# Performance work log

Measured on AMD Instinct MI355X. Metric: run time of the kernel, lower is better.

The kernel has to match this reference:

```python
import jax, jax.numpy as jnp
from jax import lax
import numpy as np

B, T_FEAT, F_DIM = 200, 2048, 128
T_CHAR, VOCAB, EMB = 128, 5000, 150
H_FEAT, H_CHAR, HID, NCLS = 256, 200, 264, 8


def gru(x, h0, W, U, b):
    """Keras GRU (v2, reset_after=True). x: [B,T,D] -> final state [B,H]."""
    xw = jnp.einsum('btd,dh->bth', x, W) + b[0]  # input projection, [B,T,3H]
    def step(h, xt):
        rec = h @ U + b[1]                        # [B,3H]
        xz, xr, xh = jnp.split(xt, 3, axis=-1)
        rz, rr, rh = jnp.split(rec, 3, axis=-1)
        z = jax.nn.sigmoid(xz + rz)
        r = jax.nn.sigmoid(xr + rr)
        hh = jnp.tanh(xh + r * rh)
        h = z * h + (1.0 - z) * hh
        return h, None
    h, _ = lax.scan(step, h0, jnp.swapaxes(xw, 0, 1))  # scan over time
    return h


def setup_inputs() -> dict:
    key = jax.random.key(0)
    ks = jax.random.split(key, 24)
    s = lambda *sh: 1.0 / np.sqrt(sh[0])
    d = {
        'numerical_inputs': jax.random.normal(ks[0], (B, 32), jnp.float32),
        'feature_inputs': jax.random.normal(ks[1], (B, T_FEAT, F_DIM), jnp.float32),
        'char_inputs': jax.random.randint(ks[2], (B, T_CHAR), 0, VOCAB, jnp.int32),
        # char embedding table (truncated-normal in orig; normal*0.01 here)
        'emb': jax.random.normal(ks[3], (VOCAB, EMB), jnp.float32) * 0.01,
        # char GRU (units=200)
        'Wc': jax.random.normal(ks[4], (EMB, 3 * H_CHAR), jnp.float32) * s(EMB),
        'Uc': jax.random.normal(ks[5], (H_CHAR, 3 * H_CHAR), jnp.float32) * s(H_CHAR),
        'bc': jnp.zeros((2, 3 * H_CHAR), jnp.float32),
        # feature GRU (units=256)
        'Wf': jax.random.normal(ks[6], (F_DIM, 3 * H_FEAT), jnp.float32) * s(F_DIM),
        'Uf': jax.random.normal(ks[7], (H_FEAT, 3 * H_FEAT), jnp.float32) * s(H_FEAT),
        'bf': jnp.zeros((2, 3 * H_FEAT), jnp.float32),
        # dense layers
        'Wfd': jax.random.normal(ks[8], (H_FEAT, HID), jnp.float32) * s(H_FEAT),
        'bfd': jnp.zeros((HID,), jnp.float32),
        'Wc1': jax.random.normal(ks[9], (H_CHAR, HID), jnp.float32) * s(H_CHAR),
        'bc1': jnp.zeros((HID,), jnp.float32),
        'Wc2': jax.random.normal(ks[10], (HID, HID), jnp.float32) * s(HID),
        'bc2': jnp.zeros((HID,), jnp.float32),
        'W1': jax.random.normal(ks[11], (2 * HID, HID), jnp.float32) * s(2 * HID),
        'b1': jnp.zeros((HID,), jnp.float32),
        'W2': jax.random.normal(ks[12], (HID, HID), jnp.float32) * s(HID),
        'b2': jnp.zeros((HID,), jnp.float32),
        'Ws': jax.random.normal(ks[13], (HID, NCLS), jnp.float32) * s(HID),
        'bs': jnp.zeros((NCLS,), jnp.float32),
    }
    return d


def reference(numerical_inputs, feature_inputs, char_inputs, emb,
              Wc, Uc, bc, Wf, Uf, bf, Wfd, bfd, Wc1, bc1, Wc2, bc2,
              W1, b1, W2, b2, Ws, bs):
    # char branch: embedding lookup -> GRU -> dense(relu) -> dense(softmax)
    e = emb[char_inputs]                                   # [B,Tc,EMB]
    hc = gru(e, jnp.zeros((e.shape[0], H_CHAR), e.dtype), Wc, Uc, bc)
    char_out = jax.nn.softmax(jax.nn.relu(hc @ Wc1 + bc1) @ Wc2 + bc2, axis=-1)
    # feature branch: GRU (dropout off / eval) -> dense(relu)
    hf = gru(feature_inputs,
             jnp.zeros((feature_inputs.shape[0], H_FEAT), feature_inputs.dtype),
             Wf, Uf, bf)
    feat_out = jax.nn.relu(hf @ Wfd + bfd)
    # fuse and classify
    x = jnp.concatenate((feat_out, char_out), axis=1)      # [B, 2*HID]
    x = jax.nn.relu(x @ W1 + b1)
    x = jax.nn.relu(x @ W2 + b2)
    return jax.nn.softmax(x @ Ws + bs, axis=-1)            # [B, 8]
```

## Files before the change

kernel.cpp:

```cpp
#include <hip/hip_runtime.h>
#include <hip/hip_bf16.h>
#include <math.h>

#define BATCH 200
#define T_FEAT 2048
#define F_DIM 128
#define T_CHAR 128
#define EMB_D 150
#define VOCAB 5000
#define H_FEAT 256
#define H_CHAR 200
#define HID 264
#define NCLS 8

#define TB 25
#define UJ 8
#define NGRP 8
#define FLAG_STRIDE 16

__global__ void prep_wt(const float* __restrict__ W, const float* __restrict__ U,
                        float* __restrict__ WT, int D, int XPAD, int H)
{
    const int DHp = XPAD + H;
    const int total = 3 * H * DHp;
    int idx = blockIdx.x * blockDim.x + threadIdx.x;
    if (idx >= total) return;
    int c = idx / DHp;
    int d = idx % DHp;
    float v;
    if (d < D)          v = W[(size_t)d * (3 * H) + c];
    else if (d < XPAD)  v = 0.f;
    else                v = U[(size_t)(d - XPAD) * (3 * H) + c];
    WT[idx] = v;
}

__global__ void prep_emb(const float* __restrict__ emb, float* __restrict__ embP)
{
    int idx = blockIdx.x * blockDim.x + threadIdx.x;
    const int total = VOCAB * 152;
    if (idx >= total) return;
    int v = idx / 152, d = idx % 152;
    embP[idx] = (d < EMB_D) ? emb[(size_t)v * EMB_D + d] : 0.f;
}

template<int XPAD, int H, int T, bool EMBED, int NBPG, int WS>
__launch_bounds__(512)
__global__ void gru_persist(const float* __restrict__ xsrc,
                            const int*   __restrict__ ids,
                            const float* __restrict__ WT,
                            const float* __restrict__ bias0,
                            const float* __restrict__ bias1,
                            float* __restrict__ hA,
                            float* __restrict__ hB,
                            unsigned* __restrict__ flags)
{
    constexpr int DHp = XPAD + H;
    constexpr int XH  = XPAD / 2;
    constexpr int HH  = H / 2;
    __shared__ float w[3 * UJ][WS];
    __shared__ float px[256 * 5];

    const int tid = threadIdx.x;
    const int bc  = blockIdx.x % NGRP;
    const int uc  = blockIdx.x / NGRP;
    const int bg  = bc * TB;
    const int ug  = uc * UJ;

    for (int i = tid; i < 3 * UJ * (DHp / 4); i += 512) {
        int r  = i / (DHp / 4);
        int d4 = (i % (DHp / 4)) * 4;
        int wrow = (r >> 3) * H + ug + (r & 7);
        *reinterpret_cast<float4*>(&w[r][d4]) =
            *reinterpret_cast<const float4*>(WT + (size_t)wrow * DHp + d4);
    }

    const int k = tid >> 8;
    const int pairIdx = tid & 255;
    const int j = pairIdx & 7;
    const int b = pairIdx >> 3;
    const bool valid = (b < TB);

    const float bzz = bias0[ug + j] + bias1[ug + j];
    const float brr = bias0[H + ug + j] + bias1[H + ug + j];
    const float bxh = bias0[2 * H + ug + j];
    const float brh = bias1[2 * H + ug + j];

    unsigned* gflags = flags + (size_t)bc * 32 * FLAG_STRIDE;
    unsigned* myflag = gflags + (size_t)uc * FLAG_STRIDE;

    float hold = 0.f;
    float xaz = 0.f, xar = 0.f, xah = 0.f;

    __syncthreads();

    if (valid) {
        const float* xrow;
        if constexpr (EMBED) {
            int id = ids[(size_t)(bg + b) * T + 0];
            xrow = xsrc + (size_t)id * XPAD + k * XH;
        } else {
            xrow = xsrc + ((size_t)(bg + b) * T + 0) * XPAD + k * XH;
        }
        const float* wz = &w[j][k * XH];
        const float* wr = &w[UJ + j][k * XH];
        const float* wh = &w[2 * UJ + j][k * XH];
        #pragma unroll 4
        for (int d = 0; d < XH; d += 4) {
            float4 xv = *reinterpret_cast<const float4*>(xrow + d);
            float4 a4 = *reinterpret_cast<const float4*>(wz + d);
            float4 c4 = *reinterpret_cast<const float4*>(wr + d);
            float4 e4 = *reinterpret_cast<const float4*>(wh + d);
            xaz += xv.x*a4.x + xv.y*a4.y + xv.z*a4.z + xv.w*a4.w;
            xar += xv.x*c4.x + xv.y*c4.y + xv.z*c4.z + xv.w*c4.w;
            xah += xv.x*e4.x + xv.y*e4.y + xv.z*e4.z + xv.w*e4.w;
        }
    }

    for (int t = 0; t < T; ++t) {
        const float* hin  = (t & 1) ? hB : hA;
        float*       hout = (t & 1) ? hA : hB;

        if (t > 0) {
            if (tid < 64) {
                const unsigned tgt = (unsigned)t;
                unsigned* fp = gflags + (size_t)tid * FLAG_STRIDE;
                const bool need = (tid < NBPG);
                for (;;) {
                    unsigned v = need ? __hip_atomic_load(fp, __ATOMIC_RELAXED,
                                                          __HIP_MEMORY_SCOPE_AGENT)
                                      : tgt;
                    if (__all((int)(v >= tgt))) break;
                }
            }
            __syncthreads();
            __builtin_amdgcn_fence(__ATOMIC_ACQUIRE, "agent");
        }

        float haz = 0.f, har = 0.f, hah = 0.f;
        if (valid) {
            const float* hrow = hin + (size_t)(bg + b) * H + k * HH;
            const float* wz = &w[j][XPAD + k * HH];
            const float* wr = &w[UJ + j][XPAD + k * HH];
            const float* wh = &w[2 * UJ + j][XPAD + k * HH];
            #pragma unroll 4
            for (int d = 0; d < HH; d += 4) {
                float4 hv = *reinterpret_cast<const float4*>(hrow + d);
                float4 a4 = *reinterpret_cast<const float4*>(wz + d);
                float4 c4 = *reinterpret_cast<const float4*>(wr + d);
                float4 e4 = *reinterpret_cast<const float4*>(wh + d);
                haz += hv.x*a4.x + hv.y*a4.y + hv.z*a4.z + hv.w*a4.w;
                har += hv.x*c4.x + hv.y*c4.y + hv.z*c4.z + hv.w*c4.w;
                hah += hv.x*e4.x + hv.y*e4.y + hv.z*e4.z + hv.w*e4.w;
            }
        }

        const float az_h = xaz + haz;
        const float ar_h = xar + har;
        if (valid && k == 1) {
            float* p = &px[pairIdx * 5];
            p[0] = az_h; p[1] = ar_h; p[2] = xah; p[3] = hah;
        }
        __syncthreads();
        if (valid && k == 0) {
            const float* p = &px[pairIdx * 5];
            float az = az_h + p[0];
            float ar = ar_h + p[1];
            float xh_t = xah + p[2];
            float rh_t = hah + p[3];
            float z = 1.f / (1.f + __expf(-(az + bzz)));
            float r = 1.f / (1.f + __expf(-(ar + brr)));
            float hh = tanhf(xh_t + bxh + r * (rh_t + brh));
            float hnew = z * hold + (1.f - z) * hh;
            hold = hnew;
            __hip_atomic_store(hout + (size_t)(bg + b) * H + ug + j, hnew,
                               __ATOMIC_RELAXED, __HIP_MEMORY_SCOPE_AGENT);
        }
        __syncthreads();
        if (tid == 0 && t + 1 < T)
            __hip_atomic_store(myflag, (unsigned)(t + 1),
                               __ATOMIC_RELAXED, __HIP_MEMORY_SCOPE_AGENT);

        xaz = xar = xah = 0.f;
        if (valid && t + 1 < T) {
            const float* xrow;
            if constexpr (EMBED) {
                int id = ids[(size_t)(bg + b) * T + (t + 1)];
                xrow = xsrc + (size_t)id * XPAD + k * XH;
            } else {
                xrow = xsrc + ((size_t)(bg + b) * T + (t + 1)) * XPAD + k * XH;
            }
            const float* wz = &w[j][k * XH];
            const float* wr = &w[UJ + j][k * XH];
            const float* wh = &w[2 * UJ + j][k * XH];
            #pragma unroll 4
            for (int d = 0; d < XH; d += 4) {
                float4 xv = *reinterpret_cast<const float4*>(xrow + d);
                float4 a4 = *reinterpret_cast<const float4*>(wz + d);
                float4 c4 = *reinterpret_cast<const float4*>(wr + d);
                float4 e4 = *reinterpret_cast<const float4*>(wh + d);
                xaz += xv.x*a4.x + xv.y*a4.y + xv.z*a4.z + xv.w*a4.w;
                xar += xv.x*c4.x + xv.y*c4.y + xv.z*c4.z + xv.w*c4.w;
                xah += xv.x*e4.x + xv.y*e4.y + xv.z*e4.z + xv.w*e4.w;
            }
        }
    }
}

template<int ACT>
__launch_bounds__(256)
__global__ void dense(const float* __restrict__ x, int ldx, int D,
                      const float* __restrict__ W, const float* __restrict__ bias, int N,
                      float* __restrict__ y, int ldy)
{
    __shared__ float xs[544];
    __shared__ float ys[288];
    __shared__ float red[2];
    const int row = blockIdx.x;
    const float* xr = x + (size_t)row * ldx;
    for (int i = threadIdx.x; i < D; i += blockDim.x) xs[i] = xr[i];
    __syncthreads();
    for (int j = threadIdx.x; j < N; j += blockDim.x) {
        float acc = bias[j];
        for (int d = 0; d < D; ++d) acc += xs[d] * W[(size_t)d * N + j];
        if (ACT == 1) acc = fmaxf(acc, 0.f);
        if (ACT == 2) ys[j] = acc;
        else          y[(size_t)row * ldy + j] = acc;
    }
    if (ACT == 2) {
        __syncthreads();
        if (threadIdx.x == 0) {
            float m = -1e30f;
            for (int i = 0; i < N; ++i) m = fmaxf(m, ys[i]);
            float s = 0.f;
            for (int i = 0; i < N; ++i) s += expf(ys[i] - m);
            red[0] = m; red[1] = s;
        }
        __syncthreads();
        float m = red[0], s = red[1];
        for (int j = threadIdx.x; j < N; j += blockDim.x)
            y[(size_t)row * ldy + j] = expf(ys[j] - m) / s;
    }
}

extern "C" void kernel_launch(void* const* d_in, const int* in_sizes, int n_in,
                              void* d_out, int out_size, void* d_ws, size_t ws_size,
                              hipStream_t stream)
{
    const float* feat = (const float*)d_in[1];
    const int*   cids = (const int*)  d_in[2];
    const float* emb  = (const float*)d_in[3];
    const float* Wc   = (const float*)d_in[4];
    const float* Uc   = (const float*)d_in[5];
    const float* bcb  = (const float*)d_in[6];
    const float* Wf   = (const float*)d_in[7];
    const float* Uf   = (const float*)d_in[8];
    const float* bfb  = (const float*)d_in[9];
    const float* Wfd  = (const float*)d_in[10]; const float* bfd = (const float*)d_in[11];
    const float* Wc1  = (const float*)d_in[12]; const float* bc1 = (const float*)d_in[13];
    const float* Wc2  = (const float*)d_in[14]; const float* bc2 = (const float*)d_in[15];
    const float* W1   = (const float*)d_in[16]; const float* b1  = (const float*)d_in[17];
    const float* W2   = (const float*)d_in[18]; const float* b2  = (const float*)d_in[19];
    const float* Wsm  = (const float*)d_in[20]; const float* bsm = (const float*)d_in[21];
    float* out = (float*)d_out;

    float* ws  = (float*)d_ws;
    float* WTf = ws; ws += 768 * 384;
    float* WTc = ws; ws += 600 * 352;
    float* embP = ws; ws += VOCAB * 152;
    float* hf0 = ws; ws += BATCH * H_FEAT;
    float* hf1 = ws; ws += BATCH * H_FEAT;
    float* hc0 = ws; ws += BATCH * H_CHAR;
    float* hc1 = ws; ws += BATCH * H_CHAR;
    float* xcat = ws; ws += BATCH * (2 * HID);
    float* tA  = ws; ws += BATCH * HID;
    float* tB  = ws; ws += BATCH * HID;
    unsigned* flagsF = (unsigned*)ws; ws += NGRP * 32 * FLAG_STRIDE;
    unsigned* flagsC = (unsigned*)ws; ws += NGRP * 32 * FLAG_STRIDE;

    hipMemsetAsync(hf0, 0, BATCH * H_FEAT * sizeof(float), stream);
    hipMemsetAsync(hc0, 0, BATCH * H_CHAR * sizeof(float), stream);
    hipMemsetAsync(flagsF, 0, NGRP * 32 * FLAG_STRIDE * sizeof(unsigned) * 2, stream);

    prep_wt<<<(768 * 384 + 255) / 256, 256, 0, stream>>>(Wf, Uf, WTf, 128, 128, H_FEAT);
    prep_wt<<<(600 * 352 + 255) / 256, 256, 0, stream>>>(Wc, Uc, WTc, 150, 152, H_CHAR);
    prep_emb<<<(VOCAB * 152 + 255) / 256, 256, 0, stream>>>(emb, embP);

    {
        const float* b0c = bcb;
        const float* b1c = bcb + 3 * H_CHAR;
        void* args[] = { (void*)&embP, (void*)&cids, (void*)&WTc, (void*)&b0c,
                         (void*)&b1c, (void*)&hc0, (void*)&hc1, (void*)&flagsC };
        hipLaunchCooperativeKernel(
            (void*)gru_persist<152, H_CHAR, T_CHAR, true, 25, 356>,
            dim3(NGRP * 25), dim3(512), args, 0, stream);
    }
    {
        const int* nullids = nullptr;
        const float* b0f = bfb;
        const float* b1f = bfb + 3 * H_FEAT;
        void* args[] = { (void*)&feat, (void*)&nullids, (void*)&WTf, (void*)&b0f,
                         (void*)&b1f, (void*)&hf0, (void*)&hf1, (void*)&flagsF };
        hipLaunchCooperativeKernel(
            (void*)gru_persist<128, H_FEAT, T_FEAT, false, 32, 388>,
            dim3(NGRP * 32), dim3(512), args, 0, stream);
    }

    dense<1><<<BATCH, 256, 0, stream>>>(hf0, H_FEAT, H_FEAT, Wfd, bfd, HID, xcat,       2 * HID);
    dense<1><<<BATCH, 256, 0, stream>>>(hc0, H_CHAR, H_CHAR, Wc1, bc1, HID, tA,         HID);
    dense<2><<<BATCH, 256, 0, stream>>>(tA,  HID,    HID,    Wc2, bc2, HID, xcat + HID, 2 * HID);
    dense<1><<<BATCH, 256, 0, stream>>>(xcat, 2 * HID, 2 * HID, W1, b1, HID, tB,        HID);
    dense<1><<<BATCH, 256, 0, stream>>>(tB,  HID,    HID,    W2,  b2,  HID, tA,         HID);
    dense<2><<<BATCH, 256, 0, stream>>>(tA,  HID,    HID,    Wsm, bsm, NCLS, out,       NCLS);
}
```

Before: 44.63 ms.

## Fuse char and feature GRU persistent kernels into one cooperative launch

Merges the two persistent GRU kernels into a single cooperative kernel. The char GRU's 128 steps run inside the first 128 iterations of the feature GRU's loop on a subset of blocks, so the serial char-GRU launch no longer sits before the feature GRU. It also register-prefetches the next feature-input row two steps ahead, adds s_sleep in the flag spin loop, and replaces tanhf with an exp-based formula. In exchange, the first 128 feature steps get longer because they also do char work and extra syncs, and the register pressure from rawF may lower occupancy.

```diff
diff --git a/kernel.cpp b/kernel.cpp
--- a/kernel.cpp
+++ b/kernel.cpp
@@ -13,9 +13,10 @@
 #define HID 264
 #define NCLS 8
 
-#define TB 25
-#define UJ 8
 #define NGRP 8
+#define TBR 25
+#define FBPG 32
+#define CBPG 25
 #define FLAG_STRIDE 16
 
 __global__ void prep_wt(const float* __restrict__ W, const float* __restrict__ U,
@@ -43,93 +44,134 @@
     embP[idx] = (d < EMB_D) ? emb[(size_t)v * EMB_D + d] : 0.f;
 }
 
-template<int XPAD, int H, int T, bool EMBED, int NBPG, int WS>
-__launch_bounds__(512)
-__global__ void gru_persist(const float* __restrict__ xsrc,
-                            const int*   __restrict__ ids,
-                            const float* __restrict__ WT,
-                            const float* __restrict__ bias0,
-                            const float* __restrict__ bias1,
-                            float* __restrict__ hA,
-                            float* __restrict__ hB,
-                            unsigned* __restrict__ flags)
+__launch_bounds__(512, 1)
+__global__ void gru_both(const float* __restrict__ feat,
+                         const int*   __restrict__ cids,
+                         const float* __restrict__ embP,
+                         const float* __restrict__ WTf,
+                         const float* __restrict__ WTc,
+                         const float* __restrict__ bf0, const float* __restrict__ bf1,
+                         const float* __restrict__ bc0, const float* __restrict__ bc1,
+                         float* __restrict__ hfA, float* __restrict__ hfB,
+                         float* __restrict__ hcA, float* __restrict__ hcB,
+                         unsigned* __restrict__ flagsF,
+                         unsigned* __restrict__ flagsC)
 {
-    constexpr int DHp = XPAD + H;
-    constexpr int XH  = XPAD / 2;
-    constexpr int HH  = H / 2;
-    __shared__ float w[3 * UJ][WS];
+    __shared__ float wF[24][388];
+    __shared__ float wC[24][356];
     __shared__ float px[256 * 5];
 
     const int tid = threadIdx.x;
-    const int bc  = blockIdx.x % NGRP;
-    const int uc  = blockIdx.x / NGRP;
-    const int bg  = bc * TB;
-    const int ug  = uc * UJ;
-
-    for (int i = tid; i < 3 * UJ * (DHp / 4); i += 512) {
-        int r  = i / (DHp / 4);
-        int d4 = (i % (DHp / 4)) * 4;
-        int wrow = (r >> 3) * H + ug + (r & 7);
-        *reinterpret_cast<float4*>(&w[r][d4]) =
-            *reinterpret_cast<const float4*>(WT + (size_t)wrow * DHp + d4);
+    const int bc  = blockIdx.x & 7;
+    const int uc  = blockIdx.x >> 3;
+    const int bg  = bc * TBR;
+    const int ugF = uc * 8;
+    const bool hasChar = (uc < CBPG);
+    const int ugC = uc * 8;
+
+    for (int i = tid; i < 24 * 96; i += 512) {
+        int r = i / 96, d4 = (i % 96) * 4;
+        int wrow = (r >> 3) * H_FEAT + ugF + (r & 7);
+        *reinterpret_cast<float4*>(&wF[r][d4]) =
+            *reinterpret_cast<const float4*>(WTf + (size_t)wrow * 384 + d4);
+    }
+    if (hasChar) {
+        for (int i = tid; i < 24 * 88; i += 512) {
+            int r = i / 88, d4 = (i % 88) * 4;
+            int wrow = (r >> 3) * H_CHAR + ugC + (r & 7);
+            *reinterpret_cast<float4*>(&wC[r][d4]) =
+                *reinterpret_cast<const float4*>(WTc + (size_t)wrow * 352 + d4);
+        }
     }
 
     const int k = tid >> 8;
     const int pairIdx = tid & 255;
     const int j = pairIdx & 7;
     const int b = pairIdx >> 3;
-    const bool valid = (b < TB);
-
-    const float bzz = bias0[ug + j] + bias1[ug + j];
-    const float brr = bias0[H + ug + j] + bias1[H + ug + j];
-    const float bxh = bias0[2 * H + ug + j];
-    const float brh = bias1[2 * H + ug + j];
-
-    unsigned* gflags = flags + (size_t)bc * 32 * FLAG_STRIDE;
-    unsigned* myflag = gflags + (size_t)uc * FLAG_STRIDE;
-
-    float hold = 0.f;
+    const bool valid = (b < TBR);
+
+    const float* wzF = wF[j];
+    const float* wrF = wF[8 + j];
+    const float* whF = wF[16 + j];
+    const float* wzC = wC[j];
+    const float* wrC = wC[8 + j];
+    const float* whC = wC[16 + j];
+
+    const float bzzF = bf0[ugF + j] + bf1[ugF + j];
+    const float brrF = bf0[H_FEAT + ugF + j] + bf1[H_FEAT + ugF + j];
+    const float bxhF = bf0[2 * H_FEAT + ugF + j];
+    const float brhF = bf1[2 * H_FEAT + ugF + j];
+    float bzzC = 0.f, brrC = 0.f, bxhC = 0.f, brhC = 0.f;
+    if (hasChar) {
+        bzzC = bc0[ugC + j] + bc1[ugC + j];
+        brrC = bc0[H_CHAR + ugC + j] + bc1[H_CHAR + ugC + j];
+        bxhC = bc0[2 * H_CHAR + ugC + j];
+        brhC = bc1[2 * H_CHAR + ugC + j];
+    }
+
+    unsigned* gfF = flagsF + (size_t)bc * 32 * FLAG_STRIDE;
+    unsigned* gfC = flagsC + (size_t)bc * 32 * FLAG_STRIDE;
+    unsigned* myF = gfF + (size_t)uc * FLAG_STRIDE;
+    unsigned* myC = gfC + (size_t)uc * FLAG_STRIDE;
+
+    __syncthreads();
+
     float xaz = 0.f, xar = 0.f, xah = 0.f;
-
-    __syncthreads();
-
+    float4 rawF[16];
     if (valid) {
-        const float* xrow;
-        if constexpr (EMBED) {
-            int id = ids[(size_t)(bg + b) * T + 0];
-            xrow = xsrc + (size_t)id * XPAD + k * XH;
-        } else {
-            xrow = xsrc + ((size_t)(bg + b) * T + 0) * XPAD + k * XH;
-        }
-        const float* wz = &w[j][k * XH];
-        const float* wr = &w[UJ + j][k * XH];
-        const float* wh = &w[2 * UJ + j][k * XH];
-        #pragma unroll 4
-        for (int d = 0; d < XH; d += 4) {
-            float4 xv = *reinterpret_cast<const float4*>(xrow + d);
-            float4 a4 = *reinterpret_cast<const float4*>(wz + d);
-            float4 c4 = *reinterpret_cast<const float4*>(wr + d);
-            float4 e4 = *reinterpret_cast<const float4*>(wh + d);
+        const float* x0 = feat + ((size_t)(bg + b) * T_FEAT + 0) * F_DIM + k * 64;
+        #pragma unroll
+        for (int i = 0; i < 16; ++i) {
+            float4 xv = reinterpret_cast<const float4*>(x0)[i];
+            float4 a4 = *reinterpret_cast<const float4*>(wzF + 4 * i + k * 64);
+            float4 c4 = *reinterpret_cast<const float4*>(wrF + 4 * i + k * 64);
+            float4 e4 = *reinterpret_cast<const float4*>(whF + 4 * i + k * 64);
             xaz += xv.x*a4.x + xv.y*a4.y + xv.z*a4.z + xv.w*a4.w;
             xar += xv.x*c4.x + xv.y*c4.y + xv.z*c4.z + xv.w*c4.w;
             xah += xv.x*e4.x + xv.y*e4.y + xv.z*e4.z + xv.w*e4.w;
         }
-    }
-
-    for (int t = 0; t < T; ++t) {
-        const float* hin  = (t & 1) ? hB : hA;
-        float*       hout = (t & 1) ? hA : hB;
+        const float* x1 = feat + ((size_t)(bg + b) * T_FEAT + 1) * F_DIM + k * 64;
+        #pragma unroll
+        for (int i = 0; i < 16; ++i) rawF[i] = reinterpret_cast<const float4*>(x1)[i];
+    }
+    float cxaz = 0.f, cxar = 0.f, cxah = 0.f;
+    if (hasChar && valid) {
+        int id0 = cids[(size_t)(bg + b) * T_CHAR + 0];
+        const float* e0 = embP + (size_t)id0 * 152 + k * 76;
+        #pragma unroll
+        for (int i = 0; i < 19; ++i) {
+            float4 xv = reinterpret_cast<const float4*>(e0)[i];
+            float4 a4 = *reinterpret_cast<const float4*>(wzC + 4 * i + k * 76);
+            float4 c4 = *reinterpret_cast<const float4*>(wrC + 4 * i + k * 76);
+            float4 e4 = *reinterpret_cast<const float4*>(whC + 4 * i + k * 76);
+            cxaz += xv.x*a4.x + xv.y*a4.y + xv.z*a4.z + xv.w*a4.w;
+            cxar += xv.x*c4.x + xv.y*c4.y + xv.z*c4.z + xv.w*c4.w;
+            cxah += xv.x*e4.x + xv.y*e4.y + xv.z*e4.z + xv.w*e4.w;
+        }
+    }
+
+    float holdF = 0.f, holdC = 0.f;
+
+    for (int t = 0; t < T_FEAT; ++t) {
+        const float* hfin = (t & 1) ? hfB : hfA;
+        float*       hfout = (t & 1) ? hfA : hfB;
+        const bool doChar = hasChar && (t < T_CHAR);
 
         if (t > 0) {
             if (tid < 64) {
                 const unsigned tgt = (unsigned)t;
-                unsigned* fp = gflags + (size_t)tid * FLAG_STRIDE;
-                const bool need = (tid < NBPG);
+                const bool needF = (tid < FBPG);
+                const bool needC = hasChar && (t < T_CHAR) &&
+                                   (tid >= 32) && (tid < 32 + CBPG);
+                unsigned* fp = needF ? (gfF + (size_t)tid * FLAG_STRIDE)
+                             : (needC ? (gfC + (size_t)(tid - 32) * FLAG_STRIDE)
+                                      : nullptr);
                 for (;;) {
-                    unsigned v = need ? __hip_atomic_load(fp, __ATOMIC_RELAXED,
-                                                          __HIP_MEMORY_SCOPE_AGENT)
-                                      : tgt;
+                    unsigned v = fp ? __hip_atomic_load(fp, __ATOMIC_RELAXED,
+                                                        __HIP_MEMORY_SCOPE_AGENT)
+                                    : tgt;
                     if (__all((int)(v >= tgt))) break;
+                    __builtin_amdgcn_s_sleep(1);
                 }
             }
             __syncthreads();
@@ -138,69 +180,125 @@
 
         float haz = 0.f, har = 0.f, hah = 0.f;
         if (valid) {
-            const float* hrow = hin + (size_t)(bg + b) * H + k * HH;
-            const float* wz = &w[j][XPAD + k * HH];
-            const float* wr = &w[UJ + j][XPAD + k * HH];
-            const float* wh = &w[2 * UJ + j][XPAD + k * HH];
+            const float* hrow = hfin + (size_t)(bg + b) * H_FEAT + k * 128;
             #pragma unroll 4
-            for (int d = 0; d < HH; d += 4) {
-                float4 hv = *reinterpret_cast<const float4*>(hrow + d);
-                float4 a4 = *reinterpret_cast<const float4*>(wz + d);
-                float4 c4 = *reinterpret_cast<const float4*>(wr + d);
-                float4 e4 = *reinterpret_cast<const float4*>(wh + d);
+            for (int i = 0; i < 32; ++i) {
+                float4 hv = reinterpret_cast<const float4*>(hrow)[i];
+                float4 a4 = *reinterpret_cast<const float4*>(wzF + 128 + k * 128 + 4 * i);
+                float4 c4 = *reinterpret_cast<const float4*>(wrF + 128 + k * 128 + 4 * i);
+                float4 e4 = *reinterpret_cast<const float4*>(whF + 128 + k * 128 + 4 * i);
                 haz += hv.x*a4.x + hv.y*a4.y + hv.z*a4.z + hv.w*a4.w;
                 har += hv.x*c4.x + hv.y*c4.y + hv.z*c4.z + hv.w*c4.w;
                 hah += hv.x*e4.x + hv.y*e4.y + hv.z*e4.z + hv.w*e4.w;
             }
         }
-
-        const float az_h = xaz + haz;
-        const float ar_h = xar + har;
+        const float azs = xaz + haz, ars = xar + har;
         if (valid && k == 1) {
             float* p = &px[pairIdx * 5];
-            p[0] = az_h; p[1] = ar_h; p[2] = xah; p[3] = hah;
+            p[0] = azs; p[1] = ars; p[2] = xah; p[3] = hah;
         }
         __syncthreads();
         if (valid && k == 0) {
             const float* p = &px[pairIdx * 5];
-            float az = az_h + p[0];
-            float ar = ar_h + p[1];
-            float xh_t = xah + p[2];
-            float rh_t = hah + p[3];
-            float z = 1.f / (1.f + __expf(-(az + bzz)));
-            float r = 1.f / (1.f + __expf(-(ar + brr)));
-            float hh = tanhf(xh_t + bxh + r * (rh_t + brh));
-            float hnew = z * hold + (1.f - z) * hh;
-            hold = hnew;
-            __hip_atomic_store(hout + (size_t)(bg + b) * H + ug + j, hnew,
+            float az = azs + p[0];
+            float ar = ars + p[1];
+            float xh = xah + p[2];
+            float rh = hah + p[3];
+            float z = 1.f / (1.f + __expf(-(az + bzzF)));
+            float r = 1.f / (1.f + __expf(-(ar + brrF)));
+            float a = xh + bxhF + r * (rh + brhF);
+            float hh = 1.f - 2.f / (1.f + __expf(2.f * a));
+            float hnew = z * holdF + (1.f - z) * hh;
+            holdF = hnew;
+            __hip_atomic_store(hfout + (size_t)(bg + b) * H_FEAT + ugF + j, hnew,
                                __ATOMIC_RELAXED, __HIP_MEMORY_SCOPE_AGENT);
         }
         __syncthreads();
-        if (tid == 0 && t + 1 < T)
-            __hip_atomic_store(myflag, (unsigned)(t + 1),
+        if (tid == 0 && t + 1 < T_FEAT)
+            __hip_atomic_store(myF, (unsigned)(t + 1),
                                __ATOMIC_RELAXED, __HIP_MEMORY_SCOPE_AGENT);
 
-        xaz = xar = xah = 0.f;
-        if (valid && t + 1 < T) {
-            const float* xrow;
-            if constexpr (EMBED) {
-                int id = ids[(size_t)(bg + b) * T + (t + 1)];
-                xrow = xsrc + (size_t)id * XPAD + k * XH;
-            } else {
-                xrow = xsrc + ((size_t)(bg + b) * T + (t + 1)) * XPAD + k * XH;
-            }
-            const float* wz = &w[j][k * XH];
-            const float* wr = &w[UJ + j][k * XH];
-            const float* wh = &w[2 * UJ + j][k * XH];
-            #pragma unroll 4
-            for (int d = 0; d < XH; d += 4) {
-                float4 xv = *reinterpret_cast<const float4*>(xrow + d);
-                float4 a4 = *reinterpret_cast<const float4*>(wz + d);
-                float4 c4 = *reinterpret_cast<const float4*>(wr + d);
-                float4 e4 = *reinterpret_cast<const float4*>(wh + d);
-                xaz += xv.x*a4.x + xv.y*a4.y + xv.z*a4.z + xv.w*a4.w;
-                xar += xv.x*c4.x + xv.y*c4.y + xv.z*c4.z + xv.w*c4.w;
-                xah += xv.x*e4.x + xv.y*e4.y + xv.z*e4.z + xv.w*e4.w;
+        if (valid && t + 1 < T_FEAT) {
+            float nz = 0.f, nr = 0.f, nh = 0.f;
+            #pragma unroll
+            for (int i = 0; i < 16; ++i) {
+                float4 xv = rawF[i];
+                float4 a4 = *reinterpret_cast<const float4*>(wzF + 4 * i + k * 64);
+                float4 c4 = *reinterpret_cast<const float4*>(wrF + 4 * i + k * 64);
+                float4 e4 = *reinterpret_cast<const float4*>(whF + 4 * i + k * 64);
+                nz += xv.x*a4.x + xv.y*a4.y + xv.z*a4.z + xv.w*a4.w;
+                nr += xv.x*c4.x + xv.y*c4.y + xv.z*c4.z + xv.w*c4.w;
+                nh += xv.x*e4.x + xv.y*e4.y + xv.z*e4.z + xv.w*e4.w;
+            }
+            xaz = nz; xar = nr; xah = nh;
+            if (t + 2 < T_FEAT) {
+                const float* xn = feat + ((size_t)(bg + b) * T_FEAT + (t + 2)) * F_DIM + k * 64;
+                #pragma unroll
+                for (int i = 0; i < 16; ++i) rawF[i] = reinterpret_cast<const float4*>(xn)[i];
+            }
+        }
+
+        if (doChar) {
+            const float* hcin = (t & 1) ? hcB : hcA;
+            float*       hcout = (t & 1) ? hcA : hcB;
+            int idN = 0;
+            if (valid && t + 1 < T_CHAR)
+                idN = cids[(size_t)(bg + b) * T_CHAR + (t + 1)];
+
+            float chaz = 0.f, char_ = 0.f, chah = 0.f;
+            if (valid) {
+                const float* hrow = hcin + (size_t)(bg + b) * H_CHAR + k * 100;
+                #pragma unroll 5
+                for (int i = 0; i < 25; ++i) {
+                    float4 hv = reinterpret_cast<const float4*>(hrow)[i];
+                    float4 a4 = *reinterpret_cast<const float4*>(wzC + 152 + k * 100 + 4 * i);
+                    float4 c4 = *reinterpret_cast<const float4*>(wrC + 152 + k * 100 + 4 * i);
+                    float4 e4 = *reinterpret_cast<const float4*>(whC + 152 + k * 100 + 4 * i);
+                    chaz  += hv.x*a4.x + hv.y*a4.y + hv.z*a4.z + hv.w*a4.w;
+                    char_ += hv.x*c4.x + hv.y*c4.y + hv.z*c4.z + hv.w*c4.w;
+                    chah  += hv.x*e4.x + hv.y*e4.y + hv.z*e4.z + hv.w*e4.w;
+                }
+            }
+            const float cazs = cxaz + chaz, cars = cxar + char_;
+            if (valid && k == 1) {
+                float* p = &px[pairIdx * 5];
+                p[0] = cazs; p[1] = cars; p[2] = cxah; p[3] = chah;
+            }
+            __syncthreads();
+            if (valid && k == 0) {
+                const float* p = &px[pairIdx * 5];
+                float az = cazs + p[0];
+                float ar = cars + p[1];
+                float xh = cxah + p[2];
+                float rh = chah + p[3];
+                float z = 1.f / (1.f + __expf(-(az + bzzC)));
+                float r = 1.f / (1.f + __expf(-(ar + brrC)));
+                float a = xh + bxhC + r * (rh + brhC);
+                float hh = 1.f - 2.f / (1.f + __expf(2.f * a));
+                float hnew = z * holdC + (1.f - z) * hh;
+                holdC = hnew;
+                __hip_atomic_store(hcout + (size_t)(bg + b) * H_CHAR + ugC + j, hnew,
+                                   __ATOMIC_RELAXED, __HIP_MEMORY_SCOPE_AGENT);
+            }
+            __syncthreads();
+            if (tid == 0 && t + 1 < T_CHAR)
+                __hip_atomic_store(myC, (unsigned)(t + 1),
+                                   __ATOMIC_RELAXED, __HIP_MEMORY_SCOPE_AGENT);
+
+            if (valid && t + 1 < T_CHAR) {
+                const float* e1 = embP + (size_t)idN * 152 + k * 76;
+                float nz = 0.f, nr = 0.f, nh = 0.f;
+                #pragma unroll
+                for (int i = 0; i < 19; ++i) {
+                    float4 xv = reinterpret_cast<const float4*>(e1)[i];
+                    float4 a4 = *reinterpret_cast<const float4*>(wzC + 4 * i + k * 76);
+                    float4 c4 = *reinterpret_cast<const float4*>(wrC + 4 * i + k * 76);
+                    float4 e4 = *reinterpret_cast<const float4*>(whC + 4 * i + k * 76);
+                    nz += xv.x*a4.x + xv.y*a4.y + xv.z*a4.z + xv.w*a4.w;
+                    nr += xv.x*c4.x + xv.y*c4.y + xv.z*c4.z + xv.w*c4.w;
+                    nh += xv.x*e4.x + xv.y*e4.y + xv.z*e4.z + xv.w*e4.w;
+                }
+                cxaz = nz; cxar = nr; cxah = nh;
             }
         }
     }
@@ -286,23 +384,17 @@
     prep_emb<<<(VOCAB * 152 + 255) / 256, 256, 0, stream>>>(emb, embP);
 
     {
+        const float* b0f = bfb;
+        const float* b1f = bfb + 3 * H_FEAT;
         const float* b0c = bcb;
         const float* b1c = bcb + 3 * H_CHAR;
-        void* args[] = { (void*)&embP, (void*)&cids, (void*)&WTc, (void*)&b0c,
-                         (void*)&b1c, (void*)&hc0, (void*)&hc1, (void*)&flagsC };
-        hipLaunchCooperativeKernel(
-            (void*)gru_persist<152, H_CHAR, T_CHAR, true, 25, 356>,
-            dim3(NGRP * 25), dim3(512), args, 0, stream);
-    }
-    {
-        const int* nullids = nullptr;
-        const float* b0f = bfb;
-        const float* b1f = bfb + 3 * H_FEAT;
-        void* args[] = { (void*)&feat, (void*)&nullids, (void*)&WTf, (void*)&b0f,
-                         (void*)&b1f, (void*)&hf0, (void*)&hf1, (void*)&flagsF };
-        hipLaunchCooperativeKernel(
-            (void*)gru_persist<128, H_FEAT, T_FEAT, false, 32, 388>,
-            dim3(NGRP * 32), dim3(512), args, 0, stream);
+        void* args[] = { (void*)&feat, (void*)&cids, (void*)&embP,
+                         (void*)&WTf, (void*)&WTc,
+                         (void*)&b0f, (void*)&b1f, (void*)&b0c, (void*)&b1c,
+                         (void*)&hf0, (void*)&hf1, (void*)&hc0, (void*)&hc1,
+                         (void*)&flagsF, (void*)&flagsC };
+        hipLaunchCooperativeKernel((void*)gru_both,
+                                   dim3(NGRP * FBPG), dim3(512), args, 0, stream);
     }
 
     dense<1><<<BATCH, 256, 0, stream>>>(hf0, H_FEAT, H_FEAT, Wfd, bfd, HID, xcat,       2 * HID);
```

Result: slower. 62.44 ms (+39.9%).
